# Performance work log

Hardware: AMD Instinct MI355X
Metric: run time of the kernel (lower is better)

## Reference

```python
import jax, jax.numpy as jnp
import numpy as np

B, RES, DIM, HEADS, WIN, HID = 1, 512, 64, 2, 8, 256
EPS = 1e-5
N = WIN * WIN

def _ln(t, w, b):
    m = t.mean(-1, keepdims=True)
    v = jnp.mean((t - m) ** 2, axis=-1, keepdims=True)
    return (t - m) * jax.lax.rsqrt(v + EPS) * w + b

def _rel_pos_index(ws):
    coords = np.stack(np.meshgrid(np.arange(ws), np.arange(ws), indexing='ij')).reshape(2, -1)
    rel = (coords[:, :, None] - coords[:, None, :]).transpose(1, 2, 0).astype(np.int64)
    rel[..., 0] += ws - 1
    rel[..., 1] += ws - 1
    rel[..., 0] *= 2 * ws - 1
    return jnp.asarray(rel.sum(-1))  # [N, N]

REL_IDX = _rel_pos_index(WIN)

def setup_inputs() -> dict:
    key = jax.random.key(0)
    ks = jax.random.split(key, 16)
    def n(k, shape, s=1.0):
        return jax.random.normal(k, shape, dtype=jnp.float32) * s
    sc = DIM ** -0.5
    return {
        'x': n(ks[0], (B, RES * RES, DIM)),
        'f': n(ks[1], (B, RES * RES, DIM)),
        'norm1_w': jnp.ones(DIM), 'norm1_b': jnp.zeros(DIM),
        'norm1f_w': jnp.ones(DIM), 'norm1f_b': jnp.zeros(DIM),
        'wq_x': n(ks[2], (DIM, DIM), sc), 'bq_x': jnp.zeros(DIM),
        'wkv_x': n(ks[3], (DIM, 2 * DIM), sc), 'bkv_x': jnp.zeros(2 * DIM),
        'wq_f': n(ks[4], (DIM, DIM), sc), 'bq_f': jnp.zeros(DIM),
        'wkv_f': n(ks[5], (DIM, 2 * DIM), sc), 'bkv_f': jnp.zeros(2 * DIM),
        'rpb': n(ks[6], ((2 * WIN - 1) ** 2, HEADS), 0.02),
        'proj_w': n(ks[7], (DIM, DIM), sc), 'proj_b': jnp.zeros(DIM),
        'norm2_w': jnp.ones(DIM), 'norm2_b': jnp.zeros(DIM),
        'fc1_w': n(ks[8], (DIM, HID), sc), 'fc1_b': jnp.zeros(HID),
        'conv_w': n(ks[9], (HID, 1, 3, 3), 0.1), 'conv_b': jnp.zeros(HID),
        'fc2_w': n(ks[10], (HID, DIM), HID ** -0.5), 'fc2_b': jnp.zeros(DIM),
    }

def _forward(x, f, norm1_w, norm1_b, norm1f_w, norm1f_b, wq_x, bq_x, wkv_x, bkv_x,
             wq_f, bq_f, wkv_f, bkv_f, rpb, proj_w, proj_b, norm2_w, norm2_b,
             fc1_w, fc1_b, conv_w, conv_b, fc2_w, fc2_b):
    H = W = RES
    C = DIM
    d = C // HEADS
    scale = d ** -0.5
    shortcut = x
    xn = _ln(x, norm1_w, norm1_b)
    fn = _ln(f, norm1f_w, norm1f_b)

    def part(t):  # [B,L,C] -> [nW, N, C] window partition
        t = t.reshape(B, H // WIN, WIN, W // WIN, WIN, C).transpose(0, 1, 3, 2, 4, 5)
        return t.reshape(-1, N, C)

    xw, fw = part(xn), part(fn)

    def qkv(t, wq, bq, wkv, bkv):
        NW = t.shape[0]
        q = (t @ wq + bq).reshape(NW, N, HEADS, d).transpose(0, 2, 1, 3)
        kv = (t @ wkv + bkv).reshape(NW, N, 2, HEADS, d)
        return q, kv[:, :, 0].transpose(0, 2, 1, 3), kv[:, :, 1].transpose(0, 2, 1, 3)

    q, k, v = qkv(xw, wq_x, bq_x, wkv_x, bkv_x)
    qf, kf, _ = qkv(fw, wq_f, bq_f, wkv_f, bkv_f)

    attn = jnp.einsum('whnd,whmd->whnm', q * scale, k)
    attn_f = jnp.einsum('whnd,whmd->whnm', qf * scale, kf)
    bias = rpb[REL_IDX.reshape(-1)].reshape(N, N, HEADS).transpose(2, 0, 1)  # [nH,N,N]
    attn = (attn + bias) * (attn_f + bias)  # joint attention
    attn = jax.nn.softmax(attn, axis=-1)
    o = jnp.einsum('whnm,whmd->whnd', attn, v).transpose(0, 2, 1, 3).reshape(-1, N, C)
    o = o @ proj_w + proj_b
    # window reverse
    o = o.reshape(B, H // WIN, W // WIN, WIN, WIN, C).transpose(0, 1, 3, 2, 4, 5).reshape(B, H * W, C)
    x = shortcut + o
    # Simple_mlp: fc1 -> depthwise 3x3 conv -> relu -> fc2
    y = _ln(x, norm2_w, norm2_b) @ fc1_w + fc1_b  # [B,L,HID]
    y = y.transpose(0, 2, 1).reshape(B, HID, H, W)
    y = jax.lax.conv_general_dilated(y, conv_w, (1, 1), 'SAME',
                                     feature_group_count=HID,
                                     dimension_numbers=('NCHW', 'OIHW', 'NCHW'))
    y = jax.nn.relu(y + conv_b[None, :, None, None])
    y = y.reshape(B, HID, H * W).transpose(0, 2, 1) @ fc2_w + fc2_b
    return x + y

def reference(x, f, norm1_w, norm1_b, norm1f_w, norm1f_b, wq_x, bq_x, wkv_x, bkv_x,
              wq_f, bq_f, wkv_f, bkv_f, rpb, proj_w, proj_b, norm2_w, norm2_b,
              fc1_w, fc1_b, conv_w, conv_b, fc2_w, fc2_b):
    return _forward(x, f, norm1_w, norm1_b, norm1f_w, norm1f_b, wq_x, bq_x, wkv_x, bkv_x,
                    wq_f, bq_f, wkv_f, bkv_f, rpb, proj_w, proj_b, norm2_w, norm2_b,
                    fc1_w, fc1_b, conv_w, conv_b, fc2_w, fc2_b)
```

## Files before the change

### kernel.cpp

```cpp
#include <hip/hip_runtime.h>

#define RES  512
#define LTOK (RES*RES)
#define DIMC 64
#define HIDC 256
#define NWIN 4096

typedef unsigned short bfu;
typedef __attribute__((ext_vector_type(8))) short s16x8;
typedef __attribute__((ext_vector_type(4))) float f32x4;

#define MFMA(a,b,c) __builtin_amdgcn_mfma_f32_16x16x32_bf16((a),(b),(c),0,0,0)

__device__ inline bfu f2bf(float f) {
    unsigned b = __float_as_uint(f);
    return (bfu)((b + 0x7FFFu + ((b >> 16) & 1u)) >> 16);
}
__device__ inline float bf2f(bfu u) { return __uint_as_float((unsigned)u << 16); }
__device__ inline ushort4 pack4(float a, float b, float c, float d) {
    ushort4 r; r.x = f2bf(a); r.y = f2bf(b); r.z = f2bf(c); r.w = f2bf(d); return r;
}

__device__ inline s16x8 fldl(const ushort* buf, int chunkbase, int rowbase, int g, int li) {
    return *(const s16x8*)&buf[((chunkbase + g) * 64 + rowbase + li) * 8];
}
__device__ inline s16x8 fldg(const ushort* w, int rowbase, int ks, int g, int li) {
    return *(const s16x8*)&w[(rowbase + li) * 64 + 32 * ks + 8 * g];
}

__device__ inline void ln_win512(const float* __restrict__ src,
                                 const float* __restrict__ lw, const float* __restrict__ lb,
                                 ushort* dsth, ushort* dstl, int wi, int wj, int tid)
{
    const int n = tid >> 3, p = tid & 7;
    const int gtok = (wi * 8 + (n >> 3)) * RES + wj * 8 + (n & 7);
    const float* rp = src + (size_t)gtok * DIMC + p * 8;
    float v[8];
    *(float4*)&v[0] = *(const float4*)&rp[0];
    *(float4*)&v[4] = *(const float4*)&rp[4];
    float s = 0.f, s2 = 0.f;
    #pragma unroll
    for (int j = 0; j < 8; ++j) { s += v[j]; s2 += v[j] * v[j]; }
    s  += __shfl_xor(s, 1);  s  += __shfl_xor(s, 2);  s  += __shfl_xor(s, 4);
    s2 += __shfl_xor(s2, 1); s2 += __shfl_xor(s2, 2); s2 += __shfl_xor(s2, 4);
    const float mean = s * 0.015625f;
    const float var  = s2 * 0.015625f - mean * mean;
    const float rs = rsqrtf(var + 1e-5f);
    float wv[8], bv[8];
    *(float4*)&wv[0] = *(const float4*)&lw[p*8+0];  *(float4*)&bv[0] = *(const float4*)&lb[p*8+0];
    *(float4*)&wv[4] = *(const float4*)&lw[p*8+4];  *(float4*)&bv[4] = *(const float4*)&lb[p*8+4];
    unsigned pkh[4], pkl[4];
    #pragma unroll
    for (int j = 0; j < 4; ++j) {
        float a = (v[2*j]   - mean) * rs * wv[2*j]   + bv[2*j];
        float b = (v[2*j+1] - mean) * rs * wv[2*j+1] + bv[2*j+1];
        bfu ha = f2bf(a), hb = f2bf(b);
        bfu la = f2bf(a - bf2f(ha)), lb2 = f2bf(b - bf2f(hb));
        pkh[j] = (unsigned)ha | ((unsigned)hb << 16);
        pkl[j] = (unsigned)la | ((unsigned)lb2 << 16);
    }
    *(int4*)&dsth[(p * 64 + n) * 8] = *(const int4*)&pkh[0];
    *(int4*)&dstl[(p * 64 + n) * 8] = *(const int4*)&pkl[0];
}

__device__ inline void ln_seq2(const float* __restrict__ src,
                               const float* __restrict__ lw, const float* __restrict__ lb,
                               ushort* dsth, ushort* dstl, int base, int tid)
{
    const int n = tid >> 2, p = tid & 3;
    const int gtok = base + n;
    const float* rp = src + (size_t)gtok * DIMC + p * 16;
    float v[16];
    *(float4*)&v[0]  = *(const float4*)&rp[0];
    *(float4*)&v[4]  = *(const float4*)&rp[4];
    *(float4*)&v[8]  = *(const float4*)&rp[8];
    *(float4*)&v[12] = *(const float4*)&rp[12];
    float s = 0.f, s2 = 0.f;
    #pragma unroll
    for (int j = 0; j < 16; ++j) { s += v[j]; s2 += v[j] * v[j]; }
    s  += __shfl_xor(s, 1);  s  += __shfl_xor(s, 2);
    s2 += __shfl_xor(s2, 1); s2 += __shfl_xor(s2, 2);
    const float mean = s * 0.015625f;
    const float var  = s2 * 0.015625f - mean * mean;
    const float rs = rsqrtf(var + 1e-5f);
    float wv[16], bv[16];
    *(float4*)&wv[0]  = *(const float4*)&lw[p*16+0];  *(float4*)&bv[0]  = *(const float4*)&lb[p*16+0];
    *(float4*)&wv[4]  = *(const float4*)&lw[p*16+4];  *(float4*)&bv[4]  = *(const float4*)&lb[p*16+4];
    *(float4*)&wv[8]  = *(const float4*)&lw[p*16+8];  *(float4*)&bv[8]  = *(const float4*)&lb[p*16+8];
    *(float4*)&wv[12] = *(const float4*)&lw[p*16+12]; *(float4*)&bv[12] = *(const float4*)&lb[p*16+12];
    unsigned pkh[8], pkl[8];
    #pragma unroll
    for (int j = 0; j < 8; ++j) {
        float a = (v[2*j]   - mean) * rs * wv[2*j]   + bv[2*j];
        float b = (v[2*j+1] - mean) * rs * wv[2*j+1] + bv[2*j+1];
        bfu ha = f2bf(a), hb = f2bf(b);
        bfu la = f2bf(a - bf2f(ha)), lb2 = f2bf(b - bf2f(hb));
        pkh[j] = (unsigned)ha | ((unsigned)hb << 16);
        pkl[j] = (unsigned)la | ((unsigned)lb2 << 16);
    }
    *(int4*)&dsth[((2*p)   * 64 + n) * 8] = *(const int4*)&pkh[0];
    *(int4*)&dsth[((2*p+1) * 64 + n) * 8] = *(const int4*)&pkh[4];
    *(int4*)&dstl[((2*p)   * 64 + n) * 8] = *(const int4*)&pkl[0];
    *(int4*)&dstl[((2*p+1) * 64 + n) * 8] = *(const int4*)&pkl[4];
}

__device__ inline void gemmT3h(const ushort* __restrict__ wTh, const ushort* __restrict__ wTl,
                               const ushort* xh, const ushort* xl,
                               const float* __restrict__ biasv,
                               ushort* dst, int w, int cth, int g, int li)
{
    const s16x8 ah0 = fldg(wTh, 16*w, 0, g, li);
    const s16x8 ah1 = fldg(wTh, 16*w, 1, g, li);
    const s16x8 al0 = fldg(wTl, 16*w, 0, g, li);
    const s16x8 al1 = fldg(wTl, 16*w, 1, g, li);
    const float4 bias = *(const float4*)&biasv[16*w + 4*g];
    #pragma unroll
    for (int c2 = 0; c2 < 2; ++c2) {
        const int ct = 2*cth + c2;
        const s16x8 bh0 = fldl(xh, 0, 16*ct, g, li);
        const s16x8 bh1 = fldl(xh, 4, 16*ct, g, li);
        const s16x8 bl0 = fldl(xl, 0, 16*ct, g, li);
        const s16x8 bl1 = fldl(xl, 4, 16*ct, g, li);
        f32x4 acc = {0.f, 0.f, 0.f, 0.f};
        acc = MFMA(al0, bh0, acc);
        acc = MFMA(al1, bh1, acc);
        acc = MFMA(ah0, bl0, acc);
        acc = MFMA(ah1, bl1, acc);
        acc = MFMA(ah0, bh0, acc);
        acc = MFMA(ah1, bh1, acc);
        *(ushort4*)&dst[((2*w + (g>>1)) * 64 + 16*ct + li) * 8 + (g&1)*4] =
            pack4(acc[0]+bias.x, acc[1]+bias.y, acc[2]+bias.z, acc[3]+bias.w);
    }
}

__device__ inline void gemmT3fh(const ushort* __restrict__ wTh, const ushort* __restrict__ wTl,
                                const ushort* xh, const ushort* xl,
                                const float* __restrict__ biasv,
                                float* dst, int w, int cth, int g, int li)
{
    const s16x8 ah0 = fldg(wTh, 16*w, 0, g, li);
    const s16x8 ah1 = fldg(wTh, 16*w, 1, g, li);
    const s16x8 al0 = fldg(wTl, 16*w, 0, g, li);
    const s16x8 al1 = fldg(wTl, 16*w, 1, g, li);
    const float4 bias = *(const float4*)&biasv[16*w + 4*g];
    #pragma unroll
    for (int c2 = 0; c2 < 2; ++c2) {
        const int ct = 2*cth + c2;
        const s16x8 bh0 = fldl(xh, 0, 16*ct, g, li);
        const s16x8 bh1 = fldl(xh, 4, 16*ct, g, li);
        const s16x8 bl0 = fldl(xl, 0, 16*ct, g, li);
        const s16x8 bl1 = fldl(xl, 4, 16*ct, g, li);
        f32x4 acc = {0.f, 0.f, 0.f, 0.f};
        acc = MFMA(al0, bh0, acc);
        acc = MFMA(al1, bh1, acc);
        acc = MFMA(ah0, bl0, acc);
        acc = MFMA(ah1, bl1, acc);
        acc = MFMA(ah0, bh0, acc);
        acc = MFMA(ah1, bh1, acc);
        float4 st = { acc[0]+bias.x, acc[1]+bias.y, acc[2]+bias.z, acc[3]+bias.w };
        *(float4*)&dst[(16*ct + li)*68 + 16*w + 4*g] = st;
    }
}

__device__ inline void gemmT3(const ushort* __restrict__ wTh, const ushort* __restrict__ wTl,
                              const ushort* xh, const ushort* xl,
                              const float* __restrict__ biasv,
                              ushort* dst, int w, int g, int li)
{
    const s16x8 ah0 = fldg(wTh, 16*w, 0, g, li);
    const s16x8 ah1 = fldg(wTh, 16*w, 1, g, li);
    const s16x8 al0 = fldg(wTl, 16*w, 0, g, li);
    const s16x8 al1 = fldg(wTl, 16*w, 1, g, li);
    const float4 bias = *(const float4*)&biasv[16*w + 4*g];
    #pragma unroll
    for (int ct = 0; ct < 4; ++ct) {
        const s16x8 bh0 = fldl(xh, 0, 16*ct, g, li);
        const s16x8 bh1 = fldl(xh, 4, 16*ct, g, li);
        const s16x8 bl0 = fldl(xl, 0, 16*ct, g, li);
        const s16x8 bl1 = fldl(xl, 4, 16*ct, g, li);
        f32x4 acc = {0.f, 0.f, 0.f, 0.f};
        acc = MFMA(al0, bh0, acc);
        acc = MFMA(al1, bh1, acc);
        acc = MFMA(ah0, bl0, acc);
        acc = MFMA(ah1, bl1, acc);
        acc = MFMA(ah0, bh0, acc);
        acc = MFMA(ah1, bh1, acc);
        *(ushort4*)&dst[((2*w + (g>>1)) * 64 + 16*ct + li) * 8 + (g&1)*4] =
            pack4(acc[0]+bias.x, acc[1]+bias.y, acc[2]+bias.z, acc[3]+bias.w);
    }
}

__global__ __launch_bounds__(256) void k_prep(
    const float* __restrict__ wqx, const float* __restrict__ wkvx,
    const float* __restrict__ wqf, const float* __restrict__ wkvf,
    const float* __restrict__ projw, const float* __restrict__ bqx,
    const float* __restrict__ bqf, const float* __restrict__ rpb,
    const float* __restrict__ fc1w, const float* __restrict__ fc2w,
    ushort* __restrict__ wb, float* __restrict__ bsc, float* __restrict__ bias2)
{
    const float scale = 0.17677669529663687f;
    int t = blockIdx.x * 256 + threadIdx.x;
    if (t < 49152) {
        int m = t >> 12, idx = t & 4095;
        int c = idx >> 6, k = idx & 63;
        int mm = m % 6;
        float val;
        switch (mm) {
            case 0:  val = wqx [k*64  + c] * scale; break;
            case 1:  val = wkvx[k*128 + c];         break;
            case 2:  val = wkvx[k*128 + 64 + c];    break;
            case 3:  val = wqf [k*64  + c] * scale; break;
            case 4:  val = wkvf[k*128 + c];         break;
            default: val = projw[k*64 + c];         break;
        }
        bfu h = f2bf(val);
        wb[m*4096 + c*64 + k] = (m < 6) ? h : f2bf(val - bf2f(h));
    } else if (t < 65536) {
        int i = t - 49152;
        int c = i >> 6, k = i & 63;
        float val = fc1w[k*HIDC + c];
        bfu h = f2bf(val);
        wb[49152 + i] = h;
        wb[65536 + i] = f2bf(val - bf2f(h));
    } else if (t < 81920) {
        int i = t - 65536;
        int c = i >> 8, k = i & 255;
        float val = fc2w[k*DIMC + c];
        bfu h = f2bf(val);
        wb[81920 + i] = h;
        wb[98304 + i] = f2bf(val - bf2f(h));
    } else if (t < 82048) {
        int i = t - 81920;
        bsc[i] = (i < 64) ? bqx[i] * scale : bqf[i-64] * scale;
    } else if (t < 90240) {
        int i = t - 82048;
        int h = i >> 12, rest = i & 4095;
        int n = rest >> 6, m2 = rest & 63;
        int idx = ((n>>3) - (m2>>3) + 7) * 15 + ((n&7) - (m2&7) + 7);
        bias2[h*4096 + rest] = rpb[idx*2 + h];
    }
}

__global__ __launch_bounds__(512, 4) void k_attn(
    const float* __restrict__ x, const float* __restrict__ f,
    const float* __restrict__ n1w, const float* __restrict__ n1b,
    const float* __restrict__ n1fw, const float* __restrict__ n1fb,
    const float* __restrict__ bkvx, const float* __restrict__ bkvf,
    const float* __restrict__ projw32, const float* __restrict__ projb,
    const ushort* __restrict__ wbufs, const float* __restrict__ bsc,
    const float* __restrict__ bias2,
    float* __restrict__ xmid)
{
    __shared__ __align__(16) unsigned char LDSRAW[75776];
    ushort* bufA   = (ushort*)(LDSRAW);
    ushort* bufAlo = (ushort*)(LDSRAW + 8192);
    ushort* bufQF  = (ushort*)(LDSRAW + 16384);
    ushort* bufKF  = (ushort*)(LDSRAW + 24576);
    ushort* bufQ   = (ushort*)(LDSRAW + 32768);
    float*  Kf32   = (float*)(LDSRAW + 40960);
    float*  Vf32   = (float*)(LDSRAW + 58368);
    float*  Pf     = (float*)(LDSRAW);
    float*  Of     = (float*)(LDSRAW + 33280);
    float*  Wlds   = (float*)(LDSRAW);

    const int tid = (int)threadIdx.x;
    const int wv = tid >> 6, lane = tid & 63, g = lane >> 4, li = lane & 15;
    const int wid = blockIdx.x, wi = wid >> 6, wj = wid & 63;
    const int w8 = wv & 3, cth = wv >> 2;

    const ushort* wqxTh  = wbufs;
    const ushort* wkxTh  = wbufs + 4096;
    const ushort* wvxTh  = wbufs + 8192;
    const ushort* wqfTh  = wbufs + 12288;
    const ushort* wkfTh  = wbufs + 16384;
    const ushort* wqxTl  = wbufs + 24576;
    const ushort* wkxTl  = wbufs + 28672;
    const ushort* wvxTl  = wbufs + 32768;
    const ushort* wqfTl  = wbufs + 36864;
    const ushort* wkfTl  = wbufs + 40960;
    const float* bqxs = bsc, * bqfs = bsc + 64;

    ln_win512(f, n1fw, n1fb, bufA, bufAlo, wi, wj, tid);
    __syncthreads();

    gemmT3h(wqfTh, wqfTl, bufA, bufAlo, bqfs, bufQF, w8, cth, g, li);
    gemmT3h(wkfTh, wkfTl, bufA, bufAlo, bkvf, bufKF, w8, cth, g, li);
    __syncthreads();

    ln_win512(x, n1w, n1b, bufA, bufAlo, wi, wj, tid);
    __syncthreads();

    gemmT3h (wqxTh, wqxTl, bufA, bufAlo, bqxs,      bufQ, w8, cth, g, li);
    gemmT3fh(wkxTh, wkxTl, bufA, bufAlo, bkvx,      Kf32, w8, cth, g, li);
    gemmT3fh(wvxTh, wvxTl, bufA, bufAlo, bkvx + 64, Vf32, w8, cth, g, li);
    __syncthreads();

    const int h2 = tid >> 8, q2 = (tid >> 2) & 63, kh = tid & 3;
    float p[16];
    float den;
    {
        float qfreg[32], qreg[32];
        #pragma unroll
        for (int cc = 0; cc < 4; ++cc) {
            const s16x8 qfv = *(const s16x8*)&bufQF[((4*h2+cc)*64 + q2)*8];
            const s16x8 qv  = *(const s16x8*)&bufQ [((4*h2+cc)*64 + q2)*8];
            #pragma unroll
            for (int j = 0; j < 8; ++j) {
                qfreg[8*cc+j] = bf2f((bfu)(unsigned short)qfv[j]);
                qreg [8*cc+j] = bf2f((bfu)(unsigned short)qv[j]);
            }
        }
        const float* brow = &bias2[h2*4096 + q2*64];
        float mx = -1e30f;
        #pragma unroll
        for (int mi = 0; mi < 16; ++mi) {
            const int m = 4*mi + kh;
            float sf = 0.f, sx = 0.f;
            #pragma unroll
            for (int cc = 0; cc < 4; ++cc) {
                const s16x8 kfv = *(const s16x8*)&bufKF[((4*h2+cc)*64 + m)*8];
                #pragma unroll
                for (int j = 0; j < 8; ++j) sf += qfreg[8*cc+j] * bf2f((bfu)(unsigned short)kfv[j]);
            }
            #pragma unroll
            for (int c4 = 0; c4 < 8; ++c4) {
                const float4 kv = *(const float4*)&Kf32[m*68 + 32*h2 + 4*c4];
                sx += qreg[4*c4+0]*kv.x + qreg[4*c4+1]*kv.y
                    + qreg[4*c4+2]*kv.z + qreg[4*c4+3]*kv.w;
            }
            const float b = brow[m];
            const float lv = (sx + b) * (sf + b);
            p[mi] = lv;
            mx = fmaxf(mx, lv);
        }
        mx = fmaxf(mx, __shfl_xor(mx, 1));
        mx = fmaxf(mx, __shfl_xor(mx, 2));
        den = 0.f;
        #pragma unroll
        for (int mi = 0; mi < 16; ++mi) {
            const float e = __expf(p[mi] - mx);
            p[mi] = e;
            den += e;
        }
        den += __shfl_xor(den, 1);
        den += __shfl_xor(den, 2);
    }
    __syncthreads();

    {
        float* srow = &Pf[h2*4160 + q2*65];
        #pragma unroll
        for (int mi = 0; mi < 16; ++mi) srow[4*mi + kh] = p[mi];
        if (kh == 0) srow[64] = den;
    }
    __syncthreads();

    {
        const int comp = wv;
        const int head = comp >> 2, quarter = comp & 3;
        const int cbase = head*32 + quarter*8;
        const int n2 = lane;
        float acc[8];
        #pragma unroll
        for (int j = 0; j < 8; ++j) acc[j] = 0.f;
        const float* prow = &Pf[head*4160 + n2*65];
        for (int m = 0; m < 64; ++m) {
            const float pv = prow[m];
            #pragma unroll
            for (int c4 = 0; c4 < 2; ++c4) {
                const float4 vv = *(const float4*)&Vf32[m*68 + cbase + 4*c4];
                acc[4*c4+0] += pv * vv.x;
                acc[4*c4+1] += pv * vv.y;
                acc[4*c4+2] += pv * vv.z;
                acc[4*c4+3] += pv * vv.w;
            }
        }
        const float inv = 1.f / prow[64];
        #pragma unroll
        for (int j4 = 0; j4 < 2; ++j4) {
            float4 st = { acc[4*j4]*inv, acc[4*j4+1]*inv, acc[4*j4+2]*inv, acc[4*j4+3]*inv };
            *(float4*)&Of[n2*68 + cbase + 4*j4] = st;
        }
    }
    __syncthreads();

    {
        const int row = tid >> 3, c = (tid & 7) * 8;
        const float4 w0 = *(const float4*)&projw32[row*64 + c];
        const float4 w1 = *(const float4*)&projw32[row*64 + c + 4];
        *(float4*)&Wlds[row*68 + c]     = w0;
        *(float4*)&Wlds[row*68 + c + 4] = w1;
    }
    __syncthreads();

    {
        const int n = tid >> 3, c0q = (tid & 7) * 8;
        float acc2[8];
        *(float4*)&acc2[0] = *(const float4*)&projb[c0q];
        *(float4*)&acc2[4] = *(const float4*)&projb[c0q + 4];
        for (int kk = 0; kk < 64; ++kk) {
            const float a = Of[n*68 + kk];
            const float* wr = Wlds + kk*68 + c0q;
            #pragma unroll
            for (int j = 0; j < 8; ++j) acc2[j] += a * wr[j];
        }
        const int gtok = (wi*8 + (n >> 3)) * RES + wj*8 + (n & 7);
        const float4 r0 = *(const float4*)&x[(size_t)gtok*DIMC + c0q];
        const float4 r1 = *(const float4*)&x[(size_t)gtok*DIMC + c0q + 4];
        float4 o0 = { acc2[0]+r0.x, acc2[1]+r0.y, acc2[2]+r0.z, acc2[3]+r0.w };
        float4 o1 = { acc2[4]+r1.x, acc2[5]+r1.y, acc2[6]+r1.z, acc2[7]+r1.w };
        *(float4*)&xmid[(size_t)gtok*DIMC + c0q]     = o0;
        *(float4*)&xmid[(size_t)gtok*DIMC + c0q + 4] = o1;
    }
}

__global__ __launch_bounds__(256) void k_fc1(
    const float* __restrict__ xm,
    const float* __restrict__ n2w, const float* __restrict__ n2b,
    const ushort* __restrict__ fc1h, const ushort* __restrict__ fc1l,
    const float* __restrict__ fc1b,
    bfu* __restrict__ y1)
{
    __shared__ __align__(16) ushort xh[4096], xl[4096];
    const int tid = (int)threadIdx.x, wv = tid >> 6, lane = tid & 63;
    const int g = lane >> 4, li = lane & 15;
    const int base = blockIdx.x * 64;

    ln_seq2(xm, n2w, n2b, xh, xl, base, tid);
    __syncthreads();

    #pragma unroll
    for (int ot = 0; ot < 4; ++ot) {
        const int chb = 64*wv + 16*ot;
        const s16x8 ah0 = fldg(fc1h, chb, 0, g, li);
        const s16x8 ah1 = fldg(fc1h, chb, 1, g, li);
        const s16x8 al0 = fldg(fc1l, chb, 0, g, li);
        const s16x8 al1 = fldg(fc1l, chb, 1, g, li);
        const float4 bb = *(const float4*)&fc1b[chb + 4*g];
        #pragma unroll
        for (int ct = 0; ct < 4; ++ct) {
            const s16x8 bh0 = fldl(xh, 0, 16*ct, g, li);
            const s16x8 bh1 = fldl(xh, 4, 16*ct, g, li);
            const s16x8 bl0 = fldl(xl, 0, 16*ct, g, li);
            const s16x8 bl1 = fldl(xl, 4, 16*ct, g, li);
            f32x4 acc = {0.f, 0.f, 0.f, 0.f};
            acc = MFMA(al0, bh0, acc);
            acc = MFMA(al1, bh1, acc);
            acc = MFMA(ah0, bl0, acc);
            acc = MFMA(ah1, bl1, acc);
            acc = MFMA(ah0, bh0, acc);
            acc = MFMA(ah1, bh1, acc);
            const int tok = base + 16*ct + li;
            *(ushort4*)&y1[(size_t)tok*HIDC + chb + 4*g] =
                pack4(acc[0]+bb.x, acc[1]+bb.y, acc[2]+bb.z, acc[3]+bb.w);
        }
    }
}

__global__ __launch_bounds__(256) void k_conv_fc2(
    const bfu* __restrict__ y1,
    const float* __restrict__ cw, const float* __restrict__ cb,
    const ushort* __restrict__ fc2h, const ushort* __restrict__ fc2l,
    const float* __restrict__ fc2b,
    float* __restrict__ xout)
{
    __shared__ float scw[2304];
    __shared__ __align__(16) ushort chH[8192], chL[8192];
    const int tid = (int)threadIdx.x, wv = tid >> 6, lane = tid & 63;
    const int g = lane >> 4, li = lane & 15;

    for (int i = tid; i < 2304; i += 256) scw[i] = cw[i];
    __syncthreads();

    const int base = blockIdx.x * 32;
    const int ch0 = lane * 4;

    float kw[4][9];
    #pragma unroll
    for (int j = 0; j < 4; ++j)
        #pragma unroll
        for (int kidx = 0; kidx < 9; ++kidx) kw[j][kidx] = scw[(ch0+j)*9 + kidx];
    const float cb0 = cb[ch0], cb1 = cb[ch0+1], cb2 = cb[ch0+2], cb3 = cb[ch0+3];

    for (int t = 0; t < 8; ++t) {
        const int tr = wv * 8 + t;
        const int tok = base + tr;
        const int hh = tok >> 9, ww = tok & 511;
        float a0 = cb0, a1 = cb1, a2 = cb2, a3 = cb3;
        #pragma unroll
        for (int dh = -1; dh <= 1; ++dh) {
            const int h2 = hh + dh;
            if (h2 < 0 || h2 >= RES) continue;
            #pragma unroll
            for (int dw = -1; dw <= 1; ++dw) {
                const int w2 = ww + dw;
                if (w2 < 0 || w2 >= RES) continue;
                const ushort4 u = *(const ushort4*)&y1[(size_t)(h2*RES + w2)*HIDC + ch0];
                const int kidx = (dh+1)*3 + (dw+1);
                a0 += bf2f(u.x) * kw[0][kidx];
                a1 += bf2f(u.y) * kw[1][kidx];
                a2 += bf2f(u.z) * kw[2][kidx];
                a3 += bf2f(u.w) * kw[3][kidx];
            }
        }
        a0 = fmaxf(a0, 0.f); a1 = fmaxf(a1, 0.f);
        a2 = fmaxf(a2, 0.f); a3 = fmaxf(a3, 0.f);
        ushort4 hi, lo;
        hi.x = f2bf(a0); lo.x = f2bf(a0 - bf2f(hi.x));
        hi.y = f2bf(a1); lo.y = f2bf(a1 - bf2f(hi.y));
        hi.z = f2bf(a2); lo.z = f2bf(a2 - bf2f(hi.z));
        hi.w = f2bf(a3); lo.w = f2bf(a3 - bf2f(hi.w));
        const int cidx = ((ch0 >> 3) * 32 + tr) * 8 + (ch0 & 7);
        *(ushort4*)&chH[cidx] = hi;
        *(ushort4*)&chL[cidx] = lo;
    }
    __syncthreads();

    {
        const int chb = 16 * wv;
        f32x4 accA = {0.f, 0.f, 0.f, 0.f};
        f32x4 accB = {0.f, 0.f, 0.f, 0.f};
        #pragma unroll
        for (int ks = 0; ks < 8; ++ks) {
            const s16x8 ah = *(const s16x8*)&fc2h[(chb + li)*256 + 32*ks + 8*g];
            const s16x8 al = *(const s16x8*)&fc2l[(chb + li)*256 + 32*ks + 8*g];
            const s16x8 bh0 = *(const s16x8*)&chH[((4*ks + g)*32 + li) * 8];
            const s16x8 bl0 = *(const s16x8*)&chL[((4*ks + g)*32 + li) * 8];
            const s16x8 bh1 = *(const s16x8*)&chH[((4*ks + g)*32 + 16 + li) * 8];
            const s16x8 bl1 = *(const s16x8*)&chL[((4*ks + g)*32 + 16 + li) * 8];
            accA = MFMA(al, bh0, accA);
            accA = MFMA(ah, bl0, accA);
            accA = MFMA(ah, bh0, accA);
            accB = MFMA(al, bh1, accB);
            accB = MFMA(ah, bl1, accB);
            accB = MFMA(ah, bh1, accB);
        }
        const float4 bb = *(const float4*)&fc2b[chb + 4*g];
        {
            const int tok = base + li;
            float4 res = *(const float4*)&xout[(size_t)tok*DIMC + chb + 4*g];
            float4 o;
            o.x = res.x + accA[0] + bb.x;
            o.y = res.y + accA[1] + bb.y;
            o.z = res.z + accA[2] + bb.z;
            o.w = res.w + accA[3] + bb.w;
            *(float4*)&xout[(size_t)tok*DIMC + chb + 4*g] = o;
        }
        {
            const int tok = base + 16 + li;
            float4 res = *(const float4*)&xout[(size_t)tok*DIMC + chb + 4*g];
            float4 o;
            o.x = res.x + accB[0] + bb.x;
            o.y = res.y + accB[1] + bb.y;
            o.z = res.z + accB[2] + bb.z;
            o.w = res.w + accB[3] + bb.w;
            *(float4*)&xout[(size_t)tok*DIMC + chb + 4*g] = o;
        }
    }
}

extern "C" void kernel_launch(void* const* d_in, const int* in_sizes, int n_in,
                              void* d_out, int out_size, void* d_ws, size_t ws_size,
                              hipStream_t stream)
{
    const float* x    = (const float*)d_in[0];
    const float* f    = (const float*)d_in[1];
    const float* n1w  = (const float*)d_in[2];
    const float* n1b  = (const float*)d_in[3];
    const float* n1fw = (const float*)d_in[4];
    const float* n1fb = (const float*)d_in[5];
    const float* wqx  = (const float*)d_in[6];
    const float* bqx  = (const float*)d_in[7];
    const float* wkvx = (const float*)d_in[8];
    const float* bkvx = (const float*)d_in[9];
    const float* wqf  = (const float*)d_in[10];
    const float* bqf  = (const float*)d_in[11];
    const float* wkvf = (const float*)d_in[12];
    const float* bkvf = (const float*)d_in[13];
    const float* rpb  = (const float*)d_in[14];
    const float* projw= (const float*)d_in[15];
    const float* projb= (const float*)d_in[16];
    const float* n2w  = (const float*)d_in[17];
    const float* n2b  = (const float*)d_in[18];
    const float* fc1w = (const float*)d_in[19];
    const float* fc1b = (const float*)d_in[20];
    const float* cw   = (const float*)d_in[21];
    const float* cb   = (const float*)d_in[22];
    const float* fc2w = (const float*)d_in[23];
    const float* fc2b = (const float*)d_in[24];
    float* out = (float*)d_out;

    bfu* y1 = (bfu*)d_ws;
    char* tb = (char*)d_ws + (size_t)LTOK * HIDC * 2;
    ushort* wb   = (ushort*)tb;
    float* bsc   = (float*)(tb + 229376);
    float* bias2 = (float*)(tb + 229888);
    float* xmid  = out;

    hipLaunchKernelGGL(k_prep, dim3(353), dim3(256), 0, stream,
                       wqx, wkvx, wqf, wkvf, projw, bqx, bqf, rpb, fc1w, fc2w,
                       wb, bsc, bias2);
    hipLaunchKernelGGL(k_attn, dim3(NWIN), dim3(512), 0, stream,
                       x, f, n1w, n1b, n1fw, n1fb, bkvx, bkvf, projw, projb,
                       wb, bsc, bias2, xmid);
    hipLaunchKernelGGL(k_fc1, dim3(LTOK/64), dim3(256), 0, stream,
                       xmid, n2w, n2b, wb + 49152, wb + 65536, fc1b, y1);
    hipLaunchKernelGGL(k_conv_fc2, dim3(LTOK/32), dim3(256), 0, stream,
                       y1, cw, cb, wb + 81920, wb + 98304, fc2b, xmid);
}
```

Measured before the change: 522.6 us.

## Fuse LayerNorm2 and fc1 GEMM into attention kernel epilogue

Removes the separate k_fc1 launch and computes norm2 plus the fc1 projection inside the attention kernel, using the projected residual values still held in registers. This avoids re-reading xmid (64 floats per token) from global memory and one kernel launch. The cost is a longer attention kernel with extra syncs and more register pressure, and y1 stores are now scattered in window order rather than contiguous token blocks.

Result: slower. 554.5 us (+6.1%).

```diff
diff --git a/kernel.cpp b/kernel.cpp
--- a/kernel.cpp
+++ b/kernel.cpp
@@ -63,47 +63,6 @@
     *(int4*)&dstl[(p * 64 + n) * 8] = *(const int4*)&pkl[0];
 }
 
-__device__ inline void ln_seq2(const float* __restrict__ src,
-                               const float* __restrict__ lw, const float* __restrict__ lb,
-                               ushort* dsth, ushort* dstl, int base, int tid)
-{
-    const int n = tid >> 2, p = tid & 3;
-    const int gtok = base + n;
-    const float* rp = src + (size_t)gtok * DIMC + p * 16;
-    float v[16];
-    *(float4*)&v[0]  = *(const float4*)&rp[0];
-    *(float4*)&v[4]  = *(const float4*)&rp[4];
-    *(float4*)&v[8]  = *(const float4*)&rp[8];
-    *(float4*)&v[12] = *(const float4*)&rp[12];
-    float s = 0.f, s2 = 0.f;
-    #pragma unroll
-    for (int j = 0; j < 16; ++j) { s += v[j]; s2 += v[j] * v[j]; }
-    s  += __shfl_xor(s, 1);  s  += __shfl_xor(s, 2);
-    s2 += __shfl_xor(s2, 1); s2 += __shfl_xor(s2, 2);
-    const float mean = s * 0.015625f;
-    const float var  = s2 * 0.015625f - mean * mean;
-    const float rs = rsqrtf(var + 1e-5f);
-    float wv[16], bv[16];
-    *(float4*)&wv[0]  = *(const float4*)&lw[p*16+0];  *(float4*)&bv[0]  = *(const float4*)&lb[p*16+0];
-    *(float4*)&wv[4]  = *(const float4*)&lw[p*16+4];  *(float4*)&bv[4]  = *(const float4*)&lb[p*16+4];
-    *(float4*)&wv[8]  = *(const float4*)&lw[p*16+8];  *(float4*)&bv[8]  = *(const float4*)&lb[p*16+8];
-    *(float4*)&wv[12] = *(const float4*)&lw[p*16+12]; *(float4*)&bv[12] = *(const float4*)&lb[p*16+12];
-    unsigned pkh[8], pkl[8];
-    #pragma unroll
-    for (int j = 0; j < 8; ++j) {
-        float a = (v[2*j]   - mean) * rs * wv[2*j]   + bv[2*j];
-        float b = (v[2*j+1] - mean) * rs * wv[2*j+1] + bv[2*j+1];
-        bfu ha = f2bf(a), hb = f2bf(b);
-        bfu la = f2bf(a - bf2f(ha)), lb2 = f2bf(b - bf2f(hb));
-        pkh[j] = (unsigned)ha | ((unsigned)hb << 16);
-        pkl[j] = (unsigned)la | ((unsigned)lb2 << 16);
-    }
-    *(int4*)&dsth[((2*p)   * 64 + n) * 8] = *(const int4*)&pkh[0];
-    *(int4*)&dsth[((2*p+1) * 64 + n) * 8] = *(const int4*)&pkh[4];
-    *(int4*)&dstl[((2*p)   * 64 + n) * 8] = *(const int4*)&pkl[0];
-    *(int4*)&dstl[((2*p+1) * 64 + n) * 8] = *(const int4*)&pkl[4];
-}
-
 __device__ inline void gemmT3h(const ushort* __restrict__ wTh, const ushort* __restrict__ wTl,
                                const ushort* xh, const ushort* xl,
                                const float* __restrict__ biasv,
@@ -159,34 +118,6 @@
         acc = MFMA(ah1, bh1, acc);
         float4 st = { acc[0]+bias.x, acc[1]+bias.y, acc[2]+bias.z, acc[3]+bias.w };
         *(float4*)&dst[(16*ct + li)*68 + 16*w + 4*g] = st;
-    }
-}
-
-__device__ inline void gemmT3(const ushort* __restrict__ wTh, const ushort* __restrict__ wTl,
-                              const ushort* xh, const ushort* xl,
-                              const float* __restrict__ biasv,
-                              ushort* dst, int w, int g, int li)
-{
-    const s16x8 ah0 = fldg(wTh, 16*w, 0, g, li);
-    const s16x8 ah1 = fldg(wTh, 16*w, 1, g, li);
-    const s16x8 al0 = fldg(wTl, 16*w, 0, g, li);
-    const s16x8 al1 = fldg(wTl, 16*w, 1, g, li);
-    const float4 bias = *(const float4*)&biasv[16*w + 4*g];
-    #pragma unroll
-    for (int ct = 0; ct < 4; ++ct) {
-        const s16x8 bh0 = fldl(xh, 0, 16*ct, g, li);
-        const s16x8 bh1 = fldl(xh, 4, 16*ct, g, li);
-        const s16x8 bl0 = fldl(xl, 0, 16*ct, g, li);
-        const s16x8 bl1 = fldl(xl, 4, 16*ct, g, li);
-        f32x4 acc = {0.f, 0.f, 0.f, 0.f};
-        acc = MFMA(al0, bh0, acc);
-        acc = MFMA(al1, bh1, acc);
-        acc = MFMA(ah0, bl0, acc);
-        acc = MFMA(ah1, bl1, acc);
-        acc = MFMA(ah0, bh0, acc);
-        acc = MFMA(ah1, bh1, acc);
-        *(ushort4*)&dst[((2*w + (g>>1)) * 64 + 16*ct + li) * 8 + (g&1)*4] =
-            pack4(acc[0]+bias.x, acc[1]+bias.y, acc[2]+bias.z, acc[3]+bias.w);
     }
 }
 
@@ -247,9 +178,12 @@
     const float* __restrict__ n1fw, const float* __restrict__ n1fb,
     const float* __restrict__ bkvx, const float* __restrict__ bkvf,
     const float* __restrict__ projw32, const float* __restrict__ projb,
+    const float* __restrict__ n2w, const float* __restrict__ n2b,
+    const ushort* __restrict__ fc1h, const ushort* __restrict__ fc1l,
+    const float* __restrict__ fc1b,
     const ushort* __restrict__ wbufs, const float* __restrict__ bsc,
     const float* __restrict__ bias2,
-    float* __restrict__ xmid)
+    float* __restrict__ xmid, bfu* __restrict__ y1)
 {
     __shared__ __align__(16) unsigned char LDSRAW[75776];
     ushort* bufA   = (ushort*)(LDSRAW);
@@ -393,56 +327,71 @@
     }
     __syncthreads();
 
-    {
-        const int n = tid >> 3, c0q = (tid & 7) * 8;
-        float acc2[8];
-        *(float4*)&acc2[0] = *(const float4*)&projb[c0q];
-        *(float4*)&acc2[4] = *(const float4*)&projb[c0q + 4];
+    const int n6 = tid >> 3, c0q = (tid & 7) * 8;
+    float xv[8];
+    {
+        *(float4*)&xv[0] = *(const float4*)&projb[c0q];
+        *(float4*)&xv[4] = *(const float4*)&projb[c0q + 4];
         for (int kk = 0; kk < 64; ++kk) {
-            const float a = Of[n*68 + kk];
+            const float a = Of[n6*68 + kk];
             const float* wr = Wlds + kk*68 + c0q;
             #pragma unroll
-            for (int j = 0; j < 8; ++j) acc2[j] += a * wr[j];
-        }
-        const int gtok = (wi*8 + (n >> 3)) * RES + wj*8 + (n & 7);
+            for (int j = 0; j < 8; ++j) xv[j] += a * wr[j];
+        }
+        const int gtok = (wi*8 + (n6 >> 3)) * RES + wj*8 + (n6 & 7);
         const float4 r0 = *(const float4*)&x[(size_t)gtok*DIMC + c0q];
         const float4 r1 = *(const float4*)&x[(size_t)gtok*DIMC + c0q + 4];
-        float4 o0 = { acc2[0]+r0.x, acc2[1]+r0.y, acc2[2]+r0.z, acc2[3]+r0.w };
-        float4 o1 = { acc2[4]+r1.x, acc2[5]+r1.y, acc2[6]+r1.z, acc2[7]+r1.w };
+        xv[0] += r0.x; xv[1] += r0.y; xv[2] += r0.z; xv[3] += r0.w;
+        xv[4] += r1.x; xv[5] += r1.y; xv[6] += r1.z; xv[7] += r1.w;
+        float4 o0 = { xv[0], xv[1], xv[2], xv[3] };
+        float4 o1 = { xv[4], xv[5], xv[6], xv[7] };
         *(float4*)&xmid[(size_t)gtok*DIMC + c0q]     = o0;
         *(float4*)&xmid[(size_t)gtok*DIMC + c0q + 4] = o1;
     }
-}
-
-__global__ __launch_bounds__(256) void k_fc1(
-    const float* __restrict__ xm,
-    const float* __restrict__ n2w, const float* __restrict__ n2b,
-    const ushort* __restrict__ fc1h, const ushort* __restrict__ fc1l,
-    const float* __restrict__ fc1b,
-    bfu* __restrict__ y1)
-{
-    __shared__ __align__(16) ushort xh[4096], xl[4096];
-    const int tid = (int)threadIdx.x, wv = tid >> 6, lane = tid & 63;
-    const int g = lane >> 4, li = lane & 15;
-    const int base = blockIdx.x * 64;
-
-    ln_seq2(xm, n2w, n2b, xh, xl, base, tid);
+    __syncthreads();
+
+    {
+        float s = 0.f, s2 = 0.f;
+        #pragma unroll
+        for (int j = 0; j < 8; ++j) { s += xv[j]; s2 += xv[j]*xv[j]; }
+        s  += __shfl_xor(s, 1);  s  += __shfl_xor(s, 2);  s  += __shfl_xor(s, 4);
+        s2 += __shfl_xor(s2, 1); s2 += __shfl_xor(s2, 2); s2 += __shfl_xor(s2, 4);
+        const float mean = s * 0.015625f;
+        const float var  = s2 * 0.015625f - mean * mean;
+        const float rs = rsqrtf(var + 1e-5f);
+        float wv2[8], bv2[8];
+        *(float4*)&wv2[0] = *(const float4*)&n2w[c0q];     *(float4*)&bv2[0] = *(const float4*)&n2b[c0q];
+        *(float4*)&wv2[4] = *(const float4*)&n2w[c0q + 4]; *(float4*)&bv2[4] = *(const float4*)&n2b[c0q + 4];
+        unsigned pkh[4], pkl[4];
+        #pragma unroll
+        for (int j = 0; j < 4; ++j) {
+            float a = (xv[2*j]   - mean) * rs * wv2[2*j]   + bv2[2*j];
+            float b = (xv[2*j+1] - mean) * rs * wv2[2*j+1] + bv2[2*j+1];
+            bfu ha = f2bf(a), hb = f2bf(b);
+            bfu la = f2bf(a - bf2f(ha)), lb2 = f2bf(b - bf2f(hb));
+            pkh[j] = (unsigned)ha | ((unsigned)hb << 16);
+            pkl[j] = (unsigned)la | ((unsigned)lb2 << 16);
+        }
+        const int pc = tid & 7;
+        *(int4*)&bufA  [(pc * 64 + n6) * 8] = *(const int4*)&pkh[0];
+        *(int4*)&bufAlo[(pc * 64 + n6) * 8] = *(const int4*)&pkl[0];
+    }
     __syncthreads();
 
     #pragma unroll
-    for (int ot = 0; ot < 4; ++ot) {
-        const int chb = 64*wv + 16*ot;
-        const s16x8 ah0 = fldg(fc1h, chb, 0, g, li);
-        const s16x8 ah1 = fldg(fc1h, chb, 1, g, li);
-        const s16x8 al0 = fldg(fc1l, chb, 0, g, li);
-        const s16x8 al1 = fldg(fc1l, chb, 1, g, li);
-        const float4 bb = *(const float4*)&fc1b[chb + 4*g];
+    for (int tt = 0; tt < 2; ++tt) {
+        const int w = wv + 8*tt;
+        const s16x8 ah0 = fldg(fc1h, 16*w, 0, g, li);
+        const s16x8 ah1 = fldg(fc1h, 16*w, 1, g, li);
+        const s16x8 al0 = fldg(fc1l, 16*w, 0, g, li);
+        const s16x8 al1 = fldg(fc1l, 16*w, 1, g, li);
+        const float4 bb = *(const float4*)&fc1b[16*w + 4*g];
         #pragma unroll
         for (int ct = 0; ct < 4; ++ct) {
-            const s16x8 bh0 = fldl(xh, 0, 16*ct, g, li);
-            const s16x8 bh1 = fldl(xh, 4, 16*ct, g, li);
-            const s16x8 bl0 = fldl(xl, 0, 16*ct, g, li);
-            const s16x8 bl1 = fldl(xl, 4, 16*ct, g, li);
+            const s16x8 bh0 = fldl(bufA,   0, 16*ct, g, li);
+            const s16x8 bh1 = fldl(bufA,   4, 16*ct, g, li);
+            const s16x8 bl0 = fldl(bufAlo, 0, 16*ct, g, li);
+            const s16x8 bl1 = fldl(bufAlo, 4, 16*ct, g, li);
             f32x4 acc = {0.f, 0.f, 0.f, 0.f};
             acc = MFMA(al0, bh0, acc);
             acc = MFMA(al1, bh1, acc);
@@ -450,8 +399,9 @@
             acc = MFMA(ah1, bl1, acc);
             acc = MFMA(ah0, bh0, acc);
             acc = MFMA(ah1, bh1, acc);
-            const int tok = base + 16*ct + li;
-            *(ushort4*)&y1[(size_t)tok*HIDC + chb + 4*g] =
+            const int nt = 16*ct + li;
+            const int gtok = (wi*8 + (nt >> 3)) * RES + wj*8 + (nt & 7);
+            *(ushort4*)&y1[(size_t)gtok*HIDC + 16*w + 4*g] =
                 pack4(acc[0]+bb.x, acc[1]+bb.y, acc[2]+bb.z, acc[3]+bb.w);
         }
     }
@@ -602,9 +552,8 @@
                        wb, bsc, bias2);
     hipLaunchKernelGGL(k_attn, dim3(NWIN), dim3(512), 0, stream,
                        x, f, n1w, n1b, n1fw, n1fb, bkvx, bkvf, projw, projb,
-                       wb, bsc, bias2, xmid);
-    hipLaunchKernelGGL(k_fc1, dim3(LTOK/64), dim3(256), 0, stream,
-                       xmid, n2w, n2b, wb + 49152, wb + 65536, fc1b, y1);
+                       n2w, n2b, wb + 49152, wb + 65536, fc1b,
+                       wb, bsc, bias2, xmid, y1);
     hipLaunchKernelGGL(k_conv_fc2, dim3(LTOK/32), dim3(256), 0, stream,
                        y1, cw, cb, wb + 81920, wb + 98304, fc2b, xmid);
 }
```
